# Kernel optimization log

Hardware: AMD Instinct MI355X
Metric: run time of the kernel (lower is better)

Reference implementation:

```python
import jax, jax.numpy as jnp
import numpy as np

B, L, T = 32, 512, 400
EMB, PRE, ENC, ARNN, DRNN, NSYM = 512, 256, 512, 1024, 1024, 256
MEAN_COEFF, SCALE_COEFF = 1.0, 10.0


def setup_inputs() -> dict:
    key = jax.random.key(0)
    ks = jax.random.split(key, 20)
    s = 0.02
    inp = {
        'memory': jax.random.normal(ks[0], (B, L, ENC), jnp.float32),
        'decoder_inputs': jax.random.normal(ks[1], (B, EMB, T), jnp.float32),
        'memory_lengths': jax.random.randint(ks[2], (B,), L // 2, L + 1).astype(jnp.int64),
        # prenet
        'pW1': jax.random.normal(ks[3], (PRE, EMB), jnp.float32) * s,
        'pb1': jnp.zeros((PRE,), jnp.float32),
        'pW2': jax.random.normal(ks[4], (PRE, PRE), jnp.float32) * s,
        'pb2': jnp.zeros((PRE,), jnp.float32),
        # attention LSTMCell
        'aWih': jax.random.normal(ks[5], (4 * ARNN, PRE + ENC), jnp.float32) * s,
        'aWhh': jax.random.normal(ks[6], (4 * ARNN, ARNN), jnp.float32) * s,
        'abih': jnp.zeros((4 * ARNN,), jnp.float32),
        'abhh': jnp.zeros((4 * ARNN,), jnp.float32),
        # Gaussian attention param linear (weight zero-init in torch; small here)
        'attWp': jax.random.normal(ks[7], (2, ARNN), jnp.float32) * 0.001,
        'attbp': jnp.zeros((2,), jnp.float32),
        # decoder LSTMCell
        'dWih': jax.random.normal(ks[8], (4 * DRNN, ARNN + ENC), jnp.float32) * s,
        'dWhh': jax.random.normal(ks[9], (4 * DRNN, DRNN), jnp.float32) * s,
        'dbih': jnp.zeros((4 * DRNN,), jnp.float32),
        'dbhh': jnp.zeros((4 * DRNN,), jnp.float32),
        # output linear
        'oW': jax.random.normal(ks[10], (NSYM, DRNN + ENC), jnp.float32) * s,
        'ob': jnp.zeros((NSYM,), jnp.float32),
    }
    return inp


def _lstm_cell(x, h, c, Wih, Whh, bih, bhh):
    g = x @ Wih.T + bih + h @ Whh.T + bhh
    i, f, gg, o = jnp.split(g, 4, axis=-1)
    c = jax.nn.sigmoid(f) * c + jax.nn.sigmoid(i) * jnp.tanh(gg)
    h = jax.nn.sigmoid(o) * jnp.tanh(c)
    return h, c


def _decoder_core(memory, decoder_inputs, memory_lengths,
                  pW1, pb1, pW2, pb2,
                  aWih, aWhh, abih, abhh,
                  attWp, attbp,
                  dWih, dWhh, dbih, dbhh,
                  oW, ob):
    b = memory.shape[0]
    Lm = memory.shape[1]
    # go frame + time-major inputs -> prenet (dropout is identity in eval)
    x = jnp.transpose(decoder_inputs, (2, 0, 1))            # [T, B, EMB]
    x = jnp.concatenate([jnp.zeros((1, b, EMB), x.dtype), x], axis=0)  # [T+1, B, EMB]
    x = jax.nn.relu(x @ pW1.T + pb1)
    x = jax.nn.relu(x @ pW2.T + pb2)                        # [T+1, B, PRE]
    x = x[:T]                                               # loop runs T steps

    lin = jnp.arange(Lm, dtype=memory.dtype)[None, :]       # [1, L]
    pad_mask = lin >= memory_lengths[:, None].astype(memory.dtype)  # [B, L] True at pad

    def step(carry, x_t):
        ah, ac, dh, dc, ctx, mean = carry
        cell_in = jnp.concatenate([x_t, ctx], axis=1)
        ah, ac = _lstm_cell(cell_in, ah, ac, aWih, aWhh, abih, abhh)
        params = ah @ attWp.T + attbp                       # [B, 2]
        mean = mean + jnp.exp(params[:, 0:1]) * MEAN_COEFF  # [B, 1]
        scale = jnp.exp(params[:, 1:2]) * SCALE_COEFF       # [B, 1]
        Z = jnp.sqrt(2.0 * np.pi * scale ** 2)
        w = jnp.exp(-0.5 * (lin - mean) ** 2 / scale ** 2) / Z  # [B, L]
        w = jnp.where(pad_mask, 0.0, w)
        ctx = jnp.einsum('bl,bld->bd', w, memory)           # [B, ENC]
        dec_in = jnp.concatenate([ah, ctx], axis=1)
        dh, dc = _lstm_cell(dec_in, dh, dc, dWih, dWhh, dbih, dbhh)
        out = jnp.concatenate([dh, ctx], axis=1) @ oW.T + ob  # [B, NSYM]
        return (ah, ac, dh, dc, ctx, mean), (out, w, params)

    z = jnp.zeros
    carry0 = (z((b, ARNN)), z((b, ARNN)), z((b, DRNN)), z((b, DRNN)),
              z((b, ENC)), z((b, 1)))
    _, (logits, aligns, ps) = jax.lax.scan(step, carry0, x)
    # time-major -> [B, T, ...]
    return (jnp.transpose(logits, (1, 0, 2)),
            jnp.transpose(aligns, (1, 0, 2)),
            jnp.transpose(ps, (1, 0, 2)))


def reference(memory, decoder_inputs, memory_lengths,
              pW1, pb1, pW2, pb2,
              aWih, aWhh, abih, abhh,
              attWp, attbp,
              dWih, dWhh, dbih, dbhh,
              oW, ob):
    return _decoder_core(memory, decoder_inputs, memory_lengths,
                         pW1, pb1, pW2, pb2,
                         aWih, aWhh, abih, abhh,
                         attWp, attbp,
                         dWih, dWhh, dbih, dbhh,
                         oW, ob)
```

## Files before the change

### kernel.cpp

```cpp
#include <hip/hip_runtime.h>
#include <math.h>

#define Bsz   32
#define Lmem  512
#define Tsteps 400
#define EMBD  512
#define PRE   256
#define ENCD  512
#define ARNN  1024
#define DRNN  1024
#define NSYM  256

typedef _Float16 f16x8 __attribute__((ext_vector_type(8)));
typedef float    f32x4 __attribute__((ext_vector_type(4)));
typedef _Float16 half_t;

#define KA  (PRE + ENCD + ARNN)
#define KAQ (KA / 4)
#define NMA (KAQ / 32)
#define KD  (ARNN + ENCD + DRNN)
#define KDQ (KD / 4)
#define NMD (KDQ / 32)
#define LDA_A 1800
#define LDA_D 2568

__device__ __forceinline__ void st_agent_f16(half_t* p, half_t v) {
    __hip_atomic_store((unsigned short*)p, __builtin_bit_cast(unsigned short, v),
                       __ATOMIC_RELAXED, __HIP_MEMORY_SCOPE_AGENT);
}
__device__ __forceinline__ void st_agent_f32(float* p, float v) {
    __hip_atomic_store(p, v, __ATOMIC_RELAXED, __HIP_MEMORY_SCOPE_AGENT);
}
__device__ __forceinline__ void st_agent_u32(unsigned* p, unsigned v) {
    __hip_atomic_store(p, v, __ATOMIC_RELAXED, __HIP_MEMORY_SCOPE_AGENT);
}
__device__ __forceinline__ void st_agent_u64(unsigned long long* p, unsigned long long v) {
    __hip_atomic_store(p, v, __ATOMIC_RELAXED, __HIP_MEMORY_SCOPE_AGENT);
}
__device__ __forceinline__ float ld_agent_f32(const float* p) {
    return __hip_atomic_load(p, __ATOMIC_RELAXED, __HIP_MEMORY_SCOPE_AGENT);
}
__device__ __forceinline__ unsigned ld_agent_u32(const unsigned* p) {
    return __hip_atomic_load(p, __ATOMIC_RELAXED, __HIP_MEMORY_SCOPE_AGENT);
}
__device__ __forceinline__ unsigned long long ld_agent_u64(const unsigned long long* p) {
    return __hip_atomic_load(p, __ATOMIC_RELAXED, __HIP_MEMORY_SCOPE_AGENT);
}
__device__ __forceinline__ f16x8 ld_agent_f16x8(const half_t* p) {
    union { unsigned long long u[2]; f16x8 v; } c;
    c.u[0] = __hip_atomic_load((const unsigned long long*)p,
                               __ATOMIC_RELAXED, __HIP_MEMORY_SCOPE_AGENT);
    c.u[1] = __hip_atomic_load(((const unsigned long long*)p) + 1,
                               __ATOMIC_RELAXED, __HIP_MEMORY_SCOPE_AGENT);
    return c.v;
}
__device__ __forceinline__ void keep16(f16x8& v) { asm volatile("" : "+v"(v)); }

template<int KIH, int KHH>
__global__ __launch_bounds__(256) void conv_lstm_w(
    const float* __restrict__ Wih, const float* __restrict__ Whh,
    const float* __restrict__ bih, const float* __restrict__ bhh,
    half_t* __restrict__ Wcat, float* __restrict__ bsum)
{
    constexpr int K = KIH + KHH;
    const int j = blockIdx.x;
    const float* srcA = Wih + (size_t)j * KIH;
    const float* srcB = Whh + (size_t)j * KHH;
    half_t* dst = Wcat + (size_t)j * K;
    for (int k = threadIdx.x; k < KIH; k += 256) dst[k]       = (half_t)srcA[k];
    for (int k = threadIdx.x; k < KHH; k += 256) dst[KIH + k] = (half_t)srcB[k];
    if (threadIdx.x == 0) bsum[j] = bih[j] + bhh[j];
}

__global__ __launch_bounds__(256) void conv_mat(
    const float* __restrict__ src, half_t* __restrict__ dst, int n)
{
    for (int i = blockIdx.x * 256 + threadIdx.x; i < n; i += gridDim.x * 256)
        dst[i] = (half_t)src[i];
}

__global__ __launch_bounds__(256) void prenet_kernel(
    const float* __restrict__ din,
    const float* __restrict__ pW1, const float* __restrict__ pb1,
    const float* __restrict__ pW2, const float* __restrict__ pb2,
    half_t* __restrict__ xpre)
{
    __shared__ float xs[8][EMBD];
    __shared__ float h1s[8][PRE];
    const int tid = threadIdx.x;
    const int row0 = blockIdx.x * 8;

    for (int idx = tid; idx < 8 * EMBD; idx += 256) {
        int r = idx >> 9;
        int e = idx & 511;
        int rid = row0 + r;
        int t = rid >> 5;
        int b = rid & 31;
        float v = 0.f;
        if (t > 0) v = din[(size_t)b * EMBD * Tsteps + (size_t)e * Tsteps + (t - 1)];
        xs[r][e] = v;
    }
    __syncthreads();

    {
        float acc[8] = {0.f,0.f,0.f,0.f,0.f,0.f,0.f,0.f};
        const float* wr = pW1 + (size_t)tid * EMBD;
        for (int e = 0; e < EMBD; e += 4) {
            float4 wv = *(const float4*)(wr + e);
            #pragma unroll
            for (int r = 0; r < 8; ++r) {
                float4 xv = *(const float4*)&xs[r][e];
                acc[r] += wv.x * xv.x + wv.y * xv.y + wv.z * xv.z + wv.w * xv.w;
            }
        }
        float bias = pb1[tid];
        #pragma unroll
        for (int r = 0; r < 8; ++r) h1s[r][tid] = fmaxf(acc[r] + bias, 0.f);
    }
    __syncthreads();

    {
        float acc[8] = {0.f,0.f,0.f,0.f,0.f,0.f,0.f,0.f};
        const float* wr = pW2 + (size_t)tid * PRE;
        for (int e = 0; e < PRE; e += 4) {
            float4 wv = *(const float4*)(wr + e);
            #pragma unroll
            for (int r = 0; r < 8; ++r) {
                float4 xv = *(const float4*)&h1s[r][e];
                acc[r] += wv.x * xv.x + wv.y * xv.y + wv.z * xv.z + wv.w * xv.w;
            }
        }
        float bias = pb2[tid];
        #pragma unroll
        for (int r = 0; r < 8; ++r) {
            int rid = row0 + r;
            int t = rid >> 5;
            int b = rid & 31;
            xpre[(size_t)t * Bsz * PRE + (size_t)b * PRE + tid] =
                (half_t)fmaxf(acc[r] + bias, 0.f);
        }
    }
}

__device__ __forceinline__ void g_arrive(unsigned* flags, unsigned ph)
{
    asm volatile("s_waitcnt vmcnt(0)" ::: "memory");
    __syncthreads();
    if (threadIdx.x == 0)
        st_agent_u32(flags + blockIdx.x * 16, ph);
}
__device__ __forceinline__ void g_wait(unsigned* flags, unsigned ph, int grp, int grank)
{
    if (grank == 0) {
        if (threadIdx.x < 32) {
            const unsigned* f = flags + (grp * 32 + threadIdx.x) * 16;
            while (ld_agent_u32(f) < ph) __builtin_amdgcn_s_sleep(1);
        }
        if (threadIdx.x == 0)
            st_agent_u32(flags + (256 + grp) * 16, ph);
        if (threadIdx.x < 8) {
            const unsigned* f2 = flags + (256 + threadIdx.x) * 16;
            while (ld_agent_u32(f2) < ph) __builtin_amdgcn_s_sleep(1);
        }
        if (threadIdx.x == 0)
            st_agent_u32(flags + (264 + grp) * 16, ph);
    } else {
        if (threadIdx.x == 0) {
            const unsigned* g = flags + (264 + grp) * 16;
            while (ld_agent_u32(g) < ph) __builtin_amdgcn_s_sleep(1);
        }
    }
    __syncthreads();
}

__global__ __launch_bounds__(512, 2) void decoder_persistent(
    const half_t* __restrict__ Wcat_a, const float* __restrict__ bsum_a,
    const half_t* __restrict__ Wcat_d, const float* __restrict__ bsum_d,
    const half_t* __restrict__ Wo, const float* __restrict__ ob,
    const half_t* __restrict__ xpre,
    const float* __restrict__ attWp, const float* __restrict__ attbp,
    const int* __restrict__ mlen, const half_t* __restrict__ mem16,
    half_t* __restrict__ ah0, half_t* __restrict__ ah1,
    half_t* __restrict__ dh0, half_t* __restrict__ dh1,
    half_t* __restrict__ ctx0, half_t* __restrict__ ctx1,
    float* __restrict__ mean0, float* __restrict__ mean1,
    float* __restrict__ partials,
    float* __restrict__ logits, float* __restrict__ aligns,
    float* __restrict__ ps,
    unsigned* flags)
{
    const int blk   = blockIdx.x;
    const int tid   = threadIdx.x;
    const int wave  = tid >> 6;
    const int lane  = tid & 63;
    const int btile = wave & 1;
    const int kq    = wave >> 1;
    const int m15   = lane & 15;
    const int kh    = lane >> 4;
    const int u0    = blk << 2;
    const int bb    = (btile << 4) + m15;
    const int grp   = blk >> 5;
    const int grank = blk & 31;

    __shared__ __align__(16) half_t wAl[16 * LDA_A];
    __shared__ __align__(16) half_t wDl[16 * LDA_D];
    __shared__ float gredA[4][2][16][16];
    __shared__ float gredD[4][2][16][16];
    __shared__ float wsh[Lmem];
    __shared__ float lred[16][33];
    __shared__ float part[4][32][2];
    __shared__ float wred8[8][2];
    __shared__ float bc2[2];

    for (int g = tid; g < 16 * (KA / 8); g += 512) {
        int r = g / (KA / 8);
        int c = (g - r * (KA / 8)) * 8;
        int jr = (r >> 2) * 1024 + u0 + (r & 3);
        *(f16x8*)(wAl + r * LDA_A + c) = *(const f16x8*)(Wcat_a + (size_t)jr * KA + c);
    }
    for (int g = tid; g < 16 * (KD / 8); g += 512) {
        int r = g / (KD / 8);
        int c = (g - r * (KD / 8)) * 8;
        int jr = (r >> 2) * 1024 + u0 + (r & 3);
        *(f16x8*)(wDl + r * LDA_D + c) = *(const f16x8*)(Wcat_d + (size_t)jr * KD + c);
    }
    float bsA[4] = {0.f,0.f,0.f,0.f}, bsD[4] = {0.f,0.f,0.f,0.f};
    float wp0 = 0.f, wp1 = 0.f;
    float cA = 0.f, cD = 0.f;
    if (tid < 128) {
        const int ul = tid >> 5;
        #pragma unroll
        for (int gi = 0; gi < 4; ++gi) bsA[gi] = bsum_a[gi * 1024 + u0 + ul];
        wp0 = attWp[u0 + ul];
        wp1 = attWp[ARNN + u0 + ul];
    } else if (tid < 256) {
        const int ul = (tid - 128) >> 5;
        #pragma unroll
        for (int gi = 0; gi < 4; ++gi) bsD[gi] = bsum_d[gi * 1024 + u0 + ul];
    }
    const half_t* lA = wAl + m15 * LDA_A + kq * KAQ + (kh << 3);
    const half_t* lD = wDl + m15 * LDA_D + kq * KDQ + (kh << 3);
    __syncthreads();

    f16x8 bvA[NMA], bvD[NMD];
    {
        const half_t* s0 = xpre;
        #pragma unroll
        for (int i = 0; i < NMA; ++i) {
            const int kg = kq * KAQ + i * 32 + (kh << 3);
            if (kg < PRE)             bvA[i] = *(const f16x8*)(s0 + bb * PRE + kg);
            else if (kg < PRE + ENCD) bvA[i] = ld_agent_f16x8(ctx1 + bb * ENCD + (kg - PRE));
            else                      bvA[i] = ld_agent_f16x8(ah1 + bb * ARNN + (kg - PRE - ENCD));
        }
    }

    unsigned ph = 0;

    for (int t = 0; t <= Tsteps + 1; ++t) {
        const int par = t & 1;
        half_t*       ah_cur  = par ? ah1 : ah0;
        half_t*       ctx_cur = par ? ctx1 : ctx0;
        float*        mn_cur  = par ? mean1 : mean0;
        const float*  mn_prv  = par ? mean0 : mean1;
        half_t*       dh_s    = par ? dh0 : dh1;
        const half_t* dh_prv  = par ? dh1 : dh0;

        if (t < Tsteps) {
            f32x4 accA = {0.f,0.f,0.f,0.f};
            #pragma unroll
            for (int i = 0; i < NMA; ++i) {
                f16x8 av = *(const f16x8*)(lA + i * 32);
                accA = __builtin_amdgcn_mfma_f32_16x16x32_f16(av, bvA[i], accA, 0, 0, 0);
            }
            #pragma unroll
            for (int r = 0; r < 4; ++r)
                gredA[kq][btile][(kh << 2) + r][m15] = accA[r];
        }
        if (t >= 1 && t <= Tsteps) {
            f32x4 accD = {0.f,0.f,0.f,0.f};
            #pragma unroll
            for (int i = 0; i < NMD; ++i) {
                f16x8 av = *(const f16x8*)(lD + i * 32);
                accD = __builtin_amdgcn_mfma_f32_16x16x32_f16(av, bvD[i], accD, 0, 0, 0);
            }
            #pragma unroll
            for (int r = 0; r < 4; ++r)
                gredD[kq][btile][(kh << 2) + r][m15] = accD[r];
        }
        if (t >= 2) {
            const int b_o = tid & 31;
            const int ks  = tid >> 5;
            const half_t* wrow = Wo + (size_t)blk * (DRNN + ENCD) + ks * 96;
            float outacc = 0.f;
            #pragma unroll
            for (int hf = 0; hf < 2; ++hf) {
                f16x8 wv[6], av[6];
                #pragma unroll
                for (int c8 = 0; c8 < 6; ++c8) {
                    const int cc = hf * 6 + c8;
                    const int k = ks * 96 + cc * 8;
                    wv[c8] = *(const f16x8*)(wrow + cc * 8);
                    const half_t* ap = (k < DRNN) ? (dh_prv + b_o * DRNN + k)
                                                  : (ctx_cur + b_o * ENCD + (k - DRNN));
                    av[c8] = ld_agent_f16x8(ap);
                }
                #pragma unroll
                for (int c8 = 0; c8 < 6; ++c8)
                    #pragma unroll
                    for (int e = 0; e < 8; ++e)
                        outacc += (float)wv[c8][e] * (float)av[c8][e];
            }
            lred[ks][b_o] = outacc;
        }
        __syncthreads();
        if (tid < 128) {
            if (t < Tsteps) {
                const int ul = tid >> 5;
                const int bq = tid & 31;
                const int bt = bq >> 4;
                const int nn = bq & 15;
                float g[4];
                #pragma unroll
                for (int gi = 0; gi < 4; ++gi) {
                    const int mr = (gi << 2) + ul;
                    g[gi] = gredA[0][bt][mr][nn] + gredA[1][bt][mr][nn]
                          + gredA[2][bt][mr][nn] + gredA[3][bt][mr][nn] + bsA[gi];
                }
                float si = 1.f / (1.f + expf(-g[0]));
                float sf = 1.f / (1.f + expf(-g[1]));
                float so = 1.f / (1.f + expf(-g[3]));
                cA = sf * cA + si * tanhf(g[2]);
                float hval = so * tanhf(cA);
                st_agent_f16(&ah_cur[bq * 1024 + u0 + ul], (half_t)hval);
                part[ul][bq][0] = hval * wp0;
                part[ul][bq][1] = hval * wp1;
            }
        } else if (tid < 256) {
            if (t >= 1 && t <= Tsteps) {
                const int lt = tid - 128;
                const int ul = lt >> 5;
                const int bq = lt & 31;
                const int bt = bq >> 4;
                const int nn = bq & 15;
                float g[4];
                #pragma unroll
                for (int gi = 0; gi < 4; ++gi) {
                    const int mr = (gi << 2) + ul;
                    g[gi] = gredD[0][bt][mr][nn] + gredD[1][bt][mr][nn]
                          + gredD[2][bt][mr][nn] + gredD[3][bt][mr][nn] + bsD[gi];
                }
                float si = 1.f / (1.f + expf(-g[0]));
                float sf = 1.f / (1.f + expf(-g[1]));
                float so = 1.f / (1.f + expf(-g[3]));
                cD = sf * cD + si * tanhf(g[2]);
                st_agent_f16(&dh_s[bq * 1024 + u0 + ul], (half_t)(so * tanhf(cD)));
            }
        } else if (tid < 288) {
            if (t >= 2) {
                const int b = tid - 256;
                float s = 0.f;
                #pragma unroll
                for (int q = 0; q < 16; ++q) s += lred[q][b];
                st_agent_f32(&logits[(size_t)b * Tsteps * NSYM + (size_t)(t - 2) * NSYM + blk],
                             s + ob[blk]);
            }
        }
        __syncthreads();
        if (tid < 32 && t < Tsteps) {
            float p0 = part[0][tid][0] + part[1][tid][0] + part[2][tid][0] + part[3][tid][0];
            float p1 = part[0][tid][1] + part[1][tid][1] + part[2][tid][1] + part[3][tid][1];
            union { float2 f; unsigned long long u; } pk;
            pk.f.x = p0; pk.f.y = p1;
            st_agent_u64((unsigned long long*)(partials + ((size_t)tid * 256 + blk) * 2), pk.u);
        }
        if (t <= Tsteps) { ++ph; g_arrive(flags, ph); g_wait(flags, ph, grp, grank); }

        if (t < Tsteps) {
            const int abt = blk >> 3;
            const int dt  = blk & 7;
            float p0 = 0.f, p1 = 0.f;
            if (tid < 256) {
                union { unsigned long long u; float2 f; } pv;
                pv.u = ld_agent_u64((const unsigned long long*)(partials + ((size_t)abt * 256 + tid) * 2));
                p0 = pv.f.x; p1 = pv.f.y;
            }
            #pragma unroll
            for (int off = 32; off > 0; off >>= 1) {
                p0 += __shfl_down(p0, off, 64);
                p1 += __shfl_down(p1, off, 64);
            }
            if (lane == 0) { wred8[wave][0] = p0; wred8[wave][1] = p1; }
            __syncthreads();
            if (tid == 0) {
                float q0 = attbp[0], q1 = attbp[1];
                #pragma unroll
                for (int w = 0; w < 8; ++w) { q0 += wred8[w][0]; q1 += wred8[w][1]; }
                float mn = ld_agent_f32(&mn_prv[abt]) + expf(q0) * 1.0f;
                float sc = expf(q1) * 10.0f;
                if (dt == 0) {
                    st_agent_f32(&mn_cur[abt], mn);
                    st_agent_f32(&ps[(size_t)abt * Tsteps * 2 + (size_t)t * 2 + 0], q0);
                    st_agent_f32(&ps[(size_t)abt * Tsteps * 2 + (size_t)t * 2 + 1], q1);
                }
                bc2[0] = mn; bc2[1] = sc;
            }
            __syncthreads();
            const float mn = bc2[0], sc = bc2[1];
            const float inv_s = 1.f / sc;
            const float coef = 0.3989422804014327f * inv_s;
            const int len = mlen[abt];
            {
                float z = ((float)tid - mn) * inv_s;
                wsh[tid] = (tid < len) ? expf(-0.5f * z * z) * coef : 0.f;
            }
            __syncthreads();
            if (tid < 64) {
                const int l = (dt << 6) + tid;
                st_agent_f32(&aligns[(size_t)abt * Tsteps * Lmem + (size_t)t * Lmem + l], wsh[l]);
            }
            int lo = (int)fmaxf(0.f, floorf(mn - 9.f * sc));
            int hi = (int)fminf((float)len, ceilf(mn + 9.f * sc) + 1.f);
            const int d8 = (dt << 6) + (wave << 3);
            const half_t* mb = mem16 + (size_t)abt * Lmem * ENCD + d8;
            float acc[8] = {0.f,0.f,0.f,0.f,0.f,0.f,0.f,0.f};
            for (int l = lo + lane; l < hi; l += 64) {
                f16x8 mv = *(const f16x8*)(mb + (size_t)l * ENCD);
                float w = wsh[l];
                #pragma unroll
                for (int j = 0; j < 8; ++j) acc[j] += w * (float)mv[j];
            }
            #pragma unroll
            for (int off = 32; off > 0; off >>= 1) {
                #pragma unroll
                for (int j = 0; j < 8; ++j) acc[j] += __shfl_down(acc[j], off, 64);
            }
            if (lane == 0) {
                #pragma unroll
                for (int j = 0; j < 4; ++j) {
                    union { unsigned u; _Float16 h[2]; } pk;
                    pk.h[0] = (_Float16)acc[2 * j];
                    pk.h[1] = (_Float16)acc[2 * j + 1];
                    st_agent_u32((unsigned*)(ctx_cur + abt * ENCD + d8 + 2 * j), pk.u);
                }
            }

            ++ph; g_arrive(flags, ph);
            if (t + 1 < Tsteps) {
                const half_t* s0n = xpre + (size_t)(t + 1) * Bsz * PRE;
                #pragma unroll
                for (int i = 0; i < NMA; ++i) {
                    const int kg = kq * KAQ + i * 32 + (kh << 3);
                    if (kg < PRE)
                        bvA[i] = *(const f16x8*)(s0n + bb * PRE + kg);
                    else if (kg >= PRE + ENCD)
                        bvA[i] = ld_agent_f16x8(ah_cur + bb * ARNN + (kg - PRE - ENCD));
                }
            }
            #pragma unroll
            for (int i = 0; i < NMD; ++i) {
                const int kg = kq * KDQ + i * 32 + (kh << 3);
                if (kg < ARNN)
                    bvD[i] = ld_agent_f16x8(ah_cur + bb * ARNN + kg);
                else if (kg >= ARNN + ENCD)
                    bvD[i] = ld_agent_f16x8(dh_s + bb * DRNN + (kg - ARNN - ENCD));
            }
            #pragma unroll
            for (int i = 0; i < NMA; ++i) keep16(bvA[i]);
            #pragma unroll
            for (int i = 0; i < NMD; ++i) keep16(bvD[i]);
            g_wait(flags, ph, grp, grank);
            if (t + 1 < Tsteps) {
                #pragma unroll
                for (int i = 0; i < NMA; ++i) {
                    const int kg = kq * KAQ + i * 32 + (kh << 3);
                    if (kg >= PRE && kg < PRE + ENCD)
                        bvA[i] = ld_agent_f16x8(ctx_cur + bb * ENCD + (kg - PRE));
                }
            }
            #pragma unroll
            for (int i = 0; i < NMD; ++i) {
                const int kg = kq * KDQ + i * 32 + (kh << 3);
                if (kg >= ARNN && kg < ARNN + ENCD)
                    bvD[i] = ld_agent_f16x8(ctx_cur + bb * ENCD + (kg - ARNN));
            }
        }
    }
}

extern "C" void kernel_launch(void* const* d_in, const int* in_sizes, int n_in,
                              void* d_out, int out_size, void* d_ws, size_t ws_size,
                              hipStream_t stream)
{
    (void)in_sizes; (void)n_in; (void)out_size; (void)ws_size;
    const float* memory = (const float*)d_in[0];
    const float* din    = (const float*)d_in[1];
    const int*   mlen   = (const int*)d_in[2];
    const float* pW1    = (const float*)d_in[3];
    const float* pb1    = (const float*)d_in[4];
    const float* pW2    = (const float*)d_in[5];
    const float* pb2    = (const float*)d_in[6];
    const float* aWih   = (const float*)d_in[7];
    const float* aWhh   = (const float*)d_in[8];
    const float* abih   = (const float*)d_in[9];
    const float* abhh   = (const float*)d_in[10];
    const float* attWp  = (const float*)d_in[11];
    const float* attbp  = (const float*)d_in[12];
    const float* dWih   = (const float*)d_in[13];
    const float* dWhh   = (const float*)d_in[14];
    const float* dbih   = (const float*)d_in[15];
    const float* dbhh   = (const float*)d_in[16];
    const float* oW     = (const float*)d_in[17];
    const float* ob     = (const float*)d_in[18];

    float* logits = (float*)d_out;
    float* aligns = logits + (size_t)Bsz * Tsteps * NSYM;
    float* ps     = aligns + (size_t)Bsz * Tsteps * Lmem;

    char* base = (char*)d_ws;
    auto alloc = [&](size_t bytes) -> char* {
        char* p = base; base += (bytes + 255) & ~(size_t)255; return p;
    };
    half_t* Wcat_a = (half_t*)alloc((size_t)4096 * KA * 2);
    half_t* Wcat_d = (half_t*)alloc((size_t)4096 * KD * 2);
    half_t* Wo     = (half_t*)alloc((size_t)NSYM * (DRNN + ENCD) * 2);
    float*  bsum_a = (float*)alloc(4096 * 4);
    float*  bsum_d = (float*)alloc(4096 * 4);
    half_t* xpre   = (half_t*)alloc((size_t)Tsteps * Bsz * PRE * 2);
    half_t* mem16  = (half_t*)alloc((size_t)Bsz * Lmem * ENCD * 2);
    half_t* ah0    = (half_t*)alloc(Bsz * ARNN * 2);
    half_t* ah1    = (half_t*)alloc(Bsz * ARNN * 2);
    half_t* dh0    = (half_t*)alloc(Bsz * DRNN * 2);
    half_t* dh1    = (half_t*)alloc(Bsz * DRNN * 2);
    half_t* ctx0   = (half_t*)alloc(Bsz * ENCD * 2);
    half_t* ctx1   = (half_t*)alloc(Bsz * ENCD * 2);
    float*  mean0  = (float*)alloc(Bsz * 4);
    float*  mean1  = (float*)alloc(Bsz * 4);
    float*  partials = (float*)alloc((size_t)Bsz * 256 * 2 * 4);
    unsigned* flags = (unsigned*)alloc(272 * 16 * 4);

    (void)hipMemsetAsync(ah1,   0, Bsz * ARNN * 2, stream);
    (void)hipMemsetAsync(dh1,   0, Bsz * DRNN * 2, stream);
    (void)hipMemsetAsync(ctx1,  0, Bsz * ENCD * 2, stream);
    (void)hipMemsetAsync(mean0, 0, Bsz * 4, stream);
    (void)hipMemsetAsync(mean1, 0, Bsz * 4, stream);
    (void)hipMemsetAsync(flags, 0, 272 * 16 * 4, stream);

    conv_lstm_w<PRE + ENCD, ARNN><<<4096, 256, 0, stream>>>(
        aWih, aWhh, abih, abhh, Wcat_a, bsum_a);
    conv_lstm_w<ARNN + ENCD, DRNN><<<4096, 256, 0, stream>>>(
        dWih, dWhh, dbih, dbhh, Wcat_d, bsum_d);
    conv_mat<<<768, 256, 0, stream>>>(oW, Wo, NSYM * (DRNN + ENCD));
    conv_mat<<<4096, 256, 0, stream>>>(memory, mem16, Bsz * Lmem * ENCD);
    prenet_kernel<<<Tsteps * Bsz / 8, 256, 0, stream>>>(din, pW1, pb1, pW2, pb2, xpre);

    decoder_persistent<<<256, 512, 0, stream>>>(
        Wcat_a, bsum_a, Wcat_d, bsum_d, Wo, ob, xpre,
        attWp, attbp, mlen, mem16,
        ah0, ah1, dh0, dh1, ctx0, ctx1, mean0, mean1, partials,
        logits, aligns, ps,
        flags);
}
```

Baseline: 14.33 ms.

## Pack LSTM activations into contiguous per-batch operand rows matching weight column order

Reorders the concatenated LSTM weight columns so the context block comes last, and replaces the separate ah/dh/ctx buffers with double-buffered contiguous activation rows [x|h|ctx] per batch. Each block stages its hidden outputs in shared memory and writes them as packed 64-bit stores, and otherwise idle threads copy the next prenet frame into the row. This lets operand loads be plain strided vector loads split into pre-barrier and post-barrier parts, removing per-element branching and narrow 16-bit atomic stores. It also swaps tanhf for an exp-based tanh, which adds some rounding differences and duplicates the context writes into both buffers.

```diff
diff --git a/kernel.cpp b/kernel.cpp
--- a/kernel.cpp
+++ b/kernel.cpp
@@ -15,19 +15,17 @@
 typedef float    f32x4 __attribute__((ext_vector_type(4)));
 typedef _Float16 half_t;
 
-#define KA  (PRE + ENCD + ARNN)
-#define KAQ (KA / 4)
-#define NMA (KAQ / 32)
-#define KD  (ARNN + ENCD + DRNN)
-#define KDQ (KD / 4)
-#define NMD (KDQ / 32)
+#define KA  1792
+#define KAQ 448
+#define NMA 14
+#define CTXA0 1280
+#define KD  2560
+#define KDQ 640
+#define NMD 20
+#define CTXD0 2048
 #define LDA_A 1800
 #define LDA_D 2568
 
-__device__ __forceinline__ void st_agent_f16(half_t* p, half_t v) {
-    __hip_atomic_store((unsigned short*)p, __builtin_bit_cast(unsigned short, v),
-                       __ATOMIC_RELAXED, __HIP_MEMORY_SCOPE_AGENT);
-}
 __device__ __forceinline__ void st_agent_f32(float* p, float v) {
     __hip_atomic_store(p, v, __ATOMIC_RELAXED, __HIP_MEMORY_SCOPE_AGENT);
 }
@@ -55,8 +53,11 @@
     return c.v;
 }
 __device__ __forceinline__ void keep16(f16x8& v) { asm volatile("" : "+v"(v)); }
-
-template<int KIH, int KHH>
+__device__ __forceinline__ float tanh_f(float x) {
+    return 1.f - 2.f / (expf(2.f * x) + 1.f);
+}
+
+template<int KIH, int KHH, int L0>
 __global__ __launch_bounds__(256) void conv_lstm_w(
     const float* __restrict__ Wih, const float* __restrict__ Whh,
     const float* __restrict__ bih, const float* __restrict__ bhh,
@@ -67,8 +68,9 @@
     const float* srcA = Wih + (size_t)j * KIH;
     const float* srcB = Whh + (size_t)j * KHH;
     half_t* dst = Wcat + (size_t)j * K;
-    for (int k = threadIdx.x; k < KIH; k += 256) dst[k]       = (half_t)srcA[k];
-    for (int k = threadIdx.x; k < KHH; k += 256) dst[KIH + k] = (half_t)srcB[k];
+    for (int k = threadIdx.x; k < L0; k += 256)        dst[k] = (half_t)srcA[k];
+    for (int k = threadIdx.x; k < KHH; k += 256)       dst[L0 + k] = (half_t)srcB[k];
+    for (int k = L0 + threadIdx.x; k < KIH; k += 256)  dst[KHH + k] = (half_t)srcA[k];
     if (threadIdx.x == 0) bsum[j] = bih[j] + bhh[j];
 }
 
@@ -77,6 +79,17 @@
 {
     for (int i = blockIdx.x * 256 + threadIdx.x; i < n; i += gridDim.x * 256)
         dst[i] = (half_t)src[i];
+}
+
+__global__ __launch_bounds__(128) void xpre0_copy(
+    const half_t* __restrict__ xpre, half_t* __restrict__ actA0)
+{
+    const int b = blockIdx.x;
+    if (threadIdx.x < 64) {
+        const unsigned long long* s = (const unsigned long long*)(xpre + b * PRE);
+        unsigned long long* d = (unsigned long long*)(actA0 + (size_t)b * KA);
+        d[threadIdx.x] = s[threadIdx.x];
+    }
 }
 
 __global__ __launch_bounds__(256) void prenet_kernel(
@@ -180,9 +193,7 @@
     const half_t* __restrict__ xpre,
     const float* __restrict__ attWp, const float* __restrict__ attbp,
     const int* __restrict__ mlen, const half_t* __restrict__ mem16,
-    half_t* __restrict__ ah0, half_t* __restrict__ ah1,
-    half_t* __restrict__ dh0, half_t* __restrict__ dh1,
-    half_t* __restrict__ ctx0, half_t* __restrict__ ctx1,
+    half_t* __restrict__ actA, half_t* __restrict__ actD,
     float* __restrict__ mean0, float* __restrict__ mean1,
     float* __restrict__ partials,
     float* __restrict__ logits, float* __restrict__ aligns,
@@ -202,6 +213,9 @@
     const int grp   = blk >> 5;
     const int grank = blk & 31;
 
+    const int preA = min(NMA, max(0, (CTXA0 - kq * KAQ) >> 5));
+    const int preD = min(NMD, max(0, (CTXD0 - kq * KDQ) >> 5));
+
     __shared__ __align__(16) half_t wAl[16 * LDA_A];
     __shared__ __align__(16) half_t wDl[16 * LDA_D];
     __shared__ float gredA[4][2][16][16];
@@ -209,6 +223,8 @@
     __shared__ float wsh[Lmem];
     __shared__ float lred[16][33];
     __shared__ float part[4][32][2];
+    __shared__ half_t hstA[4][32];
+    __shared__ half_t hstD[4][32];
     __shared__ float wred8[8][2];
     __shared__ float bc2[2];
 
@@ -244,26 +260,21 @@
 
     f16x8 bvA[NMA], bvD[NMD];
     {
-        const half_t* s0 = xpre;
+        const half_t* b0 = actA + (size_t)bb * KA + kq * KAQ + (kh << 3);
         #pragma unroll
-        for (int i = 0; i < NMA; ++i) {
-            const int kg = kq * KAQ + i * 32 + (kh << 3);
-            if (kg < PRE)             bvA[i] = *(const f16x8*)(s0 + bb * PRE + kg);
-            else if (kg < PRE + ENCD) bvA[i] = ld_agent_f16x8(ctx1 + bb * ENCD + (kg - PRE));
-            else                      bvA[i] = ld_agent_f16x8(ah1 + bb * ARNN + (kg - PRE - ENCD));
-        }
+        for (int i = 0; i < NMA; ++i) bvA[i] = *(const f16x8*)(b0 + i * 32);
     }
 
     unsigned ph = 0;
 
     for (int t = 0; t <= Tsteps + 1; ++t) {
         const int par = t & 1;
-        half_t*       ah_cur  = par ? ah1 : ah0;
-        half_t*       ctx_cur = par ? ctx1 : ctx0;
+        half_t* actA_R = actA + (size_t)(par) * Bsz * KA;
+        half_t* actA_W = actA + (size_t)(par ^ 1) * Bsz * KA;
+        half_t* actD_R = actD + (size_t)(par) * Bsz * KD;
+        half_t* actD_W = actD + (size_t)(par ^ 1) * Bsz * KD;
         float*        mn_cur  = par ? mean1 : mean0;
         const float*  mn_prv  = par ? mean0 : mean1;
-        half_t*       dh_s    = par ? dh0 : dh1;
-        const half_t* dh_prv  = par ? dh1 : dh0;
 
         if (t < Tsteps) {
             f32x4 accA = {0.f,0.f,0.f,0.f};
@@ -291,24 +302,17 @@
             const int b_o = tid & 31;
             const int ks  = tid >> 5;
             const half_t* wrow = Wo + (size_t)blk * (DRNN + ENCD) + ks * 96;
+            const half_t* dhb  = actD_R + (size_t)b_o * KD + 1024;
+            const half_t* cxb  = actD_W + (size_t)b_o * KD + 1024;
             float outacc = 0.f;
             #pragma unroll
-            for (int hf = 0; hf < 2; ++hf) {
-                f16x8 wv[6], av[6];
-                #pragma unroll
-                for (int c8 = 0; c8 < 6; ++c8) {
-                    const int cc = hf * 6 + c8;
-                    const int k = ks * 96 + cc * 8;
-                    wv[c8] = *(const f16x8*)(wrow + cc * 8);
-                    const half_t* ap = (k < DRNN) ? (dh_prv + b_o * DRNN + k)
-                                                  : (ctx_cur + b_o * ENCD + (k - DRNN));
-                    av[c8] = ld_agent_f16x8(ap);
-                }
-                #pragma unroll
-                for (int c8 = 0; c8 < 6; ++c8)
-                    #pragma unroll
-                    for (int e = 0; e < 8; ++e)
-                        outacc += (float)wv[c8][e] * (float)av[c8][e];
+            for (int cc = 0; cc < 12; ++cc) {
+                const int k = ks * 96 + cc * 8;
+                f16x8 wv = *(const f16x8*)(wrow + cc * 8);
+                f16x8 av = ld_agent_f16x8((k < DRNN ? dhb : cxb) + k);
+                #pragma unroll
+                for (int e = 0; e < 8; ++e)
+                    outacc += (float)wv[e] * (float)av[e];
             }
             lred[ks][b_o] = outacc;
         }
@@ -329,9 +333,9 @@
                 float si = 1.f / (1.f + expf(-g[0]));
                 float sf = 1.f / (1.f + expf(-g[1]));
                 float so = 1.f / (1.f + expf(-g[3]));
-                cA = sf * cA + si * tanhf(g[2]);
-                float hval = so * tanhf(cA);
-                st_agent_f16(&ah_cur[bq * 1024 + u0 + ul], (half_t)hval);
+                cA = sf * cA + si * tanh_f(g[2]);
+                float hval = so * tanh_f(cA);
+                hstA[ul][bq] = (half_t)hval;
                 part[ul][bq][0] = hval * wp0;
                 part[ul][bq][1] = hval * wp1;
             }
@@ -352,8 +356,8 @@
                 float si = 1.f / (1.f + expf(-g[0]));
                 float sf = 1.f / (1.f + expf(-g[1]));
                 float so = 1.f / (1.f + expf(-g[3]));
-                cD = sf * cD + si * tanhf(g[2]);
-                st_agent_f16(&dh_s[bq * 1024 + u0 + ul], (half_t)(so * tanhf(cD)));
+                cD = sf * cD + si * tanh_f(g[2]);
+                hstD[ul][bq] = (half_t)(so * tanh_f(cD));
             }
         } else if (tid < 288) {
             if (t >= 2) {
@@ -364,14 +368,38 @@
                 st_agent_f32(&logits[(size_t)b * Tsteps * NSYM + (size_t)(t - 2) * NSYM + blk],
                              s + ob[blk]);
             }
+        } else {
+            if (t + 1 < Tsteps) {
+                const unsigned long long* src =
+                    (const unsigned long long*)(xpre + (size_t)(t + 1) * Bsz * PRE);
+                for (int j = tid - 288; j < 2048; j += 224) {
+                    const int e = j << 2;
+                    const int b = e >> 8;
+                    const int c = e & 255;
+                    unsigned long long v = src[j];
+                    st_agent_u64((unsigned long long*)(actA_W + (size_t)b * KA + c), v);
+                }
+            }
         }
         __syncthreads();
-        if (tid < 32 && t < Tsteps) {
+        if (t < Tsteps && tid < 32) {
+            union { unsigned long long u; half_t h[4]; } pk;
+            #pragma unroll
+            for (int q = 0; q < 4; ++q) pk.h[q] = hstA[q][tid];
+            st_agent_u64((unsigned long long*)(actA_W + (size_t)tid * KA + 256 + u0), pk.u);
+            st_agent_u64((unsigned long long*)(actD_W + (size_t)tid * KD + u0), pk.u);
             float p0 = part[0][tid][0] + part[1][tid][0] + part[2][tid][0] + part[3][tid][0];
             float p1 = part[0][tid][1] + part[1][tid][1] + part[2][tid][1] + part[3][tid][1];
-            union { float2 f; unsigned long long u; } pk;
-            pk.f.x = p0; pk.f.y = p1;
-            st_agent_u64((unsigned long long*)(partials + ((size_t)tid * 256 + blk) * 2), pk.u);
+            union { float2 f; unsigned long long u; } pp;
+            pp.f.x = p0; pp.f.y = p1;
+            st_agent_u64((unsigned long long*)(partials + ((size_t)tid * 256 + blk) * 2), pp.u);
+        }
+        if (t >= 1 && t <= Tsteps && tid >= 64 && tid < 96) {
+            const int b = tid - 64;
+            union { unsigned long long u; half_t h[4]; } pk;
+            #pragma unroll
+            for (int q = 0; q < 4; ++q) pk.h[q] = hstD[q][b];
+            st_agent_u64((unsigned long long*)(actD_W + (size_t)b * KD + 1024 + u0), pk.u);
         }
         if (t <= Tsteps) { ++ph; g_arrive(flags, ph); g_wait(flags, ph, grp, grank); }
 
@@ -435,54 +463,35 @@
                 for (int j = 0; j < 8; ++j) acc[j] += __shfl_down(acc[j], off, 64);
             }
             if (lane == 0) {
-                #pragma unroll
-                for (int j = 0; j < 4; ++j) {
-                    union { unsigned u; _Float16 h[2]; } pk;
-                    pk.h[0] = (_Float16)acc[2 * j];
-                    pk.h[1] = (_Float16)acc[2 * j + 1];
-                    st_agent_u32((unsigned*)(ctx_cur + abt * ENCD + d8 + 2 * j), pk.u);
-                }
+                union { unsigned long long u; half_t h[4]; } pk0, pk1;
+                #pragma unroll
+                for (int j = 0; j < 4; ++j) { pk0.h[j] = (half_t)acc[j]; pk1.h[j] = (half_t)acc[4 + j]; }
+                st_agent_u64((unsigned long long*)(actA_W + (size_t)abt * KA + CTXA0 + d8), pk0.u);
+                st_agent_u64((unsigned long long*)(actA_W + (size_t)abt * KA + CTXA0 + d8 + 4), pk1.u);
+                st_agent_u64((unsigned long long*)(actD_W + (size_t)abt * KD + CTXD0 + d8), pk0.u);
+                st_agent_u64((unsigned long long*)(actD_W + (size_t)abt * KD + CTXD0 + d8 + 4), pk1.u);
             }
 
             ++ph; g_arrive(flags, ph);
+            const half_t* baseAW = actA_W + (size_t)bb * KA + kq * KAQ + (kh << 3);
+            const half_t* baseDW = actD_W + (size_t)bb * KD + kq * KDQ + (kh << 3);
             if (t + 1 < Tsteps) {
-                const half_t* s0n = xpre + (size_t)(t + 1) * Bsz * PRE;
-                #pragma unroll
-                for (int i = 0; i < NMA; ++i) {
-                    const int kg = kq * KAQ + i * 32 + (kh << 3);
-                    if (kg < PRE)
-                        bvA[i] = *(const f16x8*)(s0n + bb * PRE + kg);
-                    else if (kg >= PRE + ENCD)
-                        bvA[i] = ld_agent_f16x8(ah_cur + bb * ARNN + (kg - PRE - ENCD));
-                }
-            }
-            #pragma unroll
-            for (int i = 0; i < NMD; ++i) {
-                const int kg = kq * KDQ + i * 32 + (kh << 3);
-                if (kg < ARNN)
-                    bvD[i] = ld_agent_f16x8(ah_cur + bb * ARNN + kg);
-                else if (kg >= ARNN + ENCD)
-                    bvD[i] = ld_agent_f16x8(dh_s + bb * DRNN + (kg - ARNN - ENCD));
-            }
-            #pragma unroll
-            for (int i = 0; i < NMA; ++i) keep16(bvA[i]);
-            #pragma unroll
-            for (int i = 0; i < NMD; ++i) keep16(bvD[i]);
+                #pragma unroll
+                for (int i = 0; i < NMA; ++i)
+                    if (i < preA) { bvA[i] = ld_agent_f16x8(baseAW + i * 32); keep16(bvA[i]); }
+            }
+            #pragma unroll
+            for (int i = 0; i < NMD; ++i)
+                if (i < preD) { bvD[i] = ld_agent_f16x8(baseDW + i * 32); keep16(bvD[i]); }
             g_wait(flags, ph, grp, grank);
             if (t + 1 < Tsteps) {
                 #pragma unroll
-                for (int i = 0; i < NMA; ++i) {
-                    const int kg = kq * KAQ + i * 32 + (kh << 3);
-                    if (kg >= PRE && kg < PRE + ENCD)
-                        bvA[i] = ld_agent_f16x8(ctx_cur + bb * ENCD + (kg - PRE));
-                }
-            }
-            #pragma unroll
-            for (int i = 0; i < NMD; ++i) {
-                const int kg = kq * KDQ + i * 32 + (kh << 3);
-                if (kg >= ARNN && kg < ARNN + ENCD)
-                    bvD[i] = ld_agent_f16x8(ctx_cur + bb * ENCD + (kg - ARNN));
-            }
+                for (int i = 0; i < NMA; ++i)
+                    if (i >= preA) bvA[i] = ld_agent_f16x8(baseAW + i * 32);
+            }
+            #pragma unroll
+            for (int i = 0; i < NMD; ++i)
+                if (i >= preD) bvD[i] = ld_agent_f16x8(baseDW + i * 32);
         }
     }
 }
@@ -527,36 +536,32 @@
     float*  bsum_d = (float*)alloc(4096 * 4);
     half_t* xpre   = (half_t*)alloc((size_t)Tsteps * Bsz * PRE * 2);
     half_t* mem16  = (half_t*)alloc((size_t)Bsz * Lmem * ENCD * 2);
-    half_t* ah0    = (half_t*)alloc(Bsz * ARNN * 2);
-    half_t* ah1    = (half_t*)alloc(Bsz * ARNN * 2);
-    half_t* dh0    = (half_t*)alloc(Bsz * DRNN * 2);
-    half_t* dh1    = (half_t*)alloc(Bsz * DRNN * 2);
-    half_t* ctx0   = (half_t*)alloc(Bsz * ENCD * 2);
-    half_t* ctx1   = (half_t*)alloc(Bsz * ENCD * 2);
+    half_t* actA   = (half_t*)alloc((size_t)2 * Bsz * KA * 2);
+    half_t* actD   = (half_t*)alloc((size_t)2 * Bsz * KD * 2);
     float*  mean0  = (float*)alloc(Bsz * 4);
     float*  mean1  = (float*)alloc(Bsz * 4);
     float*  partials = (float*)alloc((size_t)Bsz * 256 * 2 * 4);
-    unsigned* flags = (unsigned*)alloc(272 * 16 * 4);
-
-    (void)hipMemsetAsync(ah1,   0, Bsz * ARNN * 2, stream);
-    (void)hipMemsetAsync(dh1,   0, Bsz * DRNN * 2, stream);
-    (void)hipMemsetAsync(ctx1,  0, Bsz * ENCD * 2, stream);
+    unsigned* flags  = (unsigned*)alloc(272 * 16 * 4);
+
+    (void)hipMemsetAsync(actA, 0, (size_t)2 * Bsz * KA * 2, stream);
+    (void)hipMemsetAsync(actD, 0, (size_t)2 * Bsz * KD * 2, stream);
     (void)hipMemsetAsync(mean0, 0, Bsz * 4, stream);
     (void)hipMemsetAsync(mean1, 0, Bsz * 4, stream);
     (void)hipMemsetAsync(flags, 0, 272 * 16 * 4, stream);
 
-    conv_lstm_w<PRE + ENCD, ARNN><<<4096, 256, 0, stream>>>(
+    conv_lstm_w<PRE + ENCD, ARNN, PRE><<<4096, 256, 0, stream>>>(
         aWih, aWhh, abih, abhh, Wcat_a, bsum_a);
-    conv_lstm_w<ARNN + ENCD, DRNN><<<4096, 256, 0, stream>>>(
+    conv_lstm_w<ARNN + ENCD, DRNN, ARNN><<<4096, 256, 0, stream>>>(
         dWih, dWhh, dbih, dbhh, Wcat_d, bsum_d);
     conv_mat<<<768, 256, 0, stream>>>(oW, Wo, NSYM * (DRNN + ENCD));
     conv_mat<<<4096, 256, 0, stream>>>(memory, mem16, Bsz * Lmem * ENCD);
     prenet_kernel<<<Tsteps * Bsz / 8, 256, 0, stream>>>(din, pW1, pb1, pW2, pb2, xpre);
+    xpre0_copy<<<32, 128, 0, stream>>>(xpre, actA);
 
     decoder_persistent<<<256, 512, 0, stream>>>(
         Wcat_a, bsum_a, Wcat_d, bsum_d, Wo, ob, xpre,
         attWp, attbp, mlen, mem16,
-        ah0, ah1, dh0, dh1, ctx0, ctx1, mean0, mean1, partials,
+        actA, actD, mean0, mean1, partials,
         logits, aligns, ps,
         flags);
 }
```

Result: slower. 18.72 ms (+30.7%).
